# Optimization experiments

Hardware: AMD Instinct MI355X
Metric: run time of the kernel (lower is better)

Reference implementation:

```python
import jax, jax.numpy as jnp
import numpy as np

B, N, C, H = 2, 2048, 1024, 16
D = C // H  # head dim = 64
SCALE = 1.0 / (C ** 0.5)  # note: source scales by 1/sqrt(dim), not 1/sqrt(head_dim)


def setup_inputs() -> dict:
    key = jax.random.key(0)
    k1, k2, k3 = jax.random.split(key, 3)
    x = jax.random.normal(k1, (B, N, C), dtype=jnp.float32)
    w_qkv = jax.random.normal(k2, (3 * C, C), dtype=jnp.float32) * (1.0 / np.sqrt(C))
    w_proj = jax.random.normal(k3, (C, C), dtype=jnp.float32) * (1.0 / np.sqrt(C))
    b_proj = jnp.zeros((C,), dtype=jnp.float32)
    return {"x": x, "w_qkv": w_qkv, "w_proj": w_proj, "b_proj": b_proj}


def reference(x, w_qkv, w_proj, b_proj):
    Bb, Nn, Cc = x.shape
    # qkv projection (torch Linear: x @ W.T), then split into q,k,v heads
    qkv = jnp.einsum('bnc,dc->bnd', x, w_qkv)           # [B,N,3C]
    qkv = qkv.reshape(Bb, Nn, 3, H, D)
    q = qkv[:, :, 0].transpose(0, 2, 1, 3)              # [B,H,N,D]
    k = qkv[:, :, 1].transpose(0, 2, 1, 3)
    v = qkv[:, :, 2].transpose(0, 2, 1, 3)
    attn = jnp.einsum('bhnd,bhmd->bhnm', q, k) * SCALE  # [B,H,N,N]
    attn = jax.nn.softmax(attn, axis=-1)
    out = jnp.einsum('bhnm,bhmd->bhnd', attn, v)        # [B,H,N,D]
    out = out.transpose(0, 2, 1, 3).reshape(Bb, Nn, Cc)
    out = jnp.einsum('bnc,dc->bnd', out, w_proj) + b_proj
    return (out, attn)
```

## Files before the change

kernel.cpp:

```cpp
#include <hip/hip_runtime.h>

typedef __attribute__((ext_vector_type(8))) short short8;
typedef __attribute__((ext_vector_type(4))) float f32x4;
typedef __attribute__((ext_vector_type(16))) float f32x16;

#define B_ 2
#define N_ 2048
#define C_ 1024
#define H_ 16
#define SCALE_ 0.03125f

__device__ inline unsigned short f2bf(float f) {
    unsigned int u = __float_as_uint(f);
    return (unsigned short)((u + 0x7fffu + ((u >> 16) & 1u)) >> 16);
}

__device__ inline f32x4 mfma16(short8 a, short8 b, f32x4 c) {
    return __builtin_amdgcn_mfma_f32_16x16x32_bf16(a, b, c, 0, 0, 0);
}
__device__ inline f32x16 mfma32(short8 a, short8 b, f32x16 c) {
    return __builtin_amdgcn_mfma_f32_32x32x16_bf16(a, b, c, 0, 0, 0);
}

#define GLOAD_LDS16(g, l) __builtin_amdgcn_global_load_lds( \
    (const __attribute__((address_space(1))) void*)(g),     \
    (__attribute__((address_space(3))) void*)(l), 16, 0, 0)

__global__ void cvt_all(const float* __restrict__ x, const float* __restrict__ wq,
                        const float* __restrict__ wp, unsigned short* __restrict__ xb,
                        unsigned short* __restrict__ wqb, unsigned short* __restrict__ wpb) {
    int i = blockIdx.x * blockDim.x + threadIdx.x;
    const int n1 = 4096 * 1024 / 4, n2 = 3072 * 1024 / 4;
    const float* src; unsigned short* dst; int j;
    if (i < n1)            { src = x;  dst = xb;  j = i; }
    else if (i < n1 + n2)  { src = wq; dst = wqb; j = i - n1; }
    else                   { src = wp; dst = wpb; j = i - n1 - n2; }
    float4 v = *(const float4*)(src + (size_t)j * 4);
    ushort4 o;
    o.x = f2bf(v.x); o.y = f2bf(v.y); o.z = f2bf(v.z); o.w = f2bf(v.w);
    *(ushort4*)(dst + (size_t)j * 4) = o;
}

template<int BF16_OUT, int BM>
__global__ __launch_bounds__(256, 3)
void gemm_bt(const unsigned short* __restrict__ A, const unsigned short* __restrict__ Bm,
             unsigned short* __restrict__ Cb, float* __restrict__ Cf,
             const float* __restrict__ bias, int M, int N, int K,
             int xcd_cols, int bxr) {
    constexpr int AI = BM / 32;
    __shared__ unsigned short lA[BM * 64];
    __shared__ unsigned short lB[128 * 64];
    const int tid = threadIdx.x;
    const int lane = tid & 63, wave = tid >> 6;
    const int lm = lane & 15, g = lane >> 4;
    const int flat = blockIdx.x, per = gridDim.x >> 3;
    const int xcd = flat & 7, fl = flat >> 3;
    const int rpr = per / bxr;
    const int by = (xcd / xcd_cols) * rpr + fl / bxr;
    const int bx = (xcd % xcd_cols) * bxr + fl % bxr;
    const int m0 = by * BM, n0 = bx * 128;
    const int wr = wave >> 1, wc = wave & 1;

    f32x4 acc[AI][4];
    f32x4 zero = {0.f, 0.f, 0.f, 0.f};
#pragma unroll
    for (int i = 0; i < AI; ++i)
#pragma unroll
        for (int j = 0; j < 4; ++j) acc[i][j] = zero;

    const int sRow = lane >> 3;
    const int sCol = (lane & 7) * 8;

    for (int k0 = 0; k0 < K; k0 += 64) {
#pragma unroll
        for (int t = 0; t < AI; ++t) {
            int inst = wave * AI + t;
            int r = inst * 8 + sRow;
            GLOAD_LDS16(A + (size_t)(m0 + r) * K + k0 + sCol, lA + inst * 512);
        }
#pragma unroll
        for (int t = 0; t < 4; ++t) {
            int inst = wave * 4 + t;
            int r = inst * 8 + sRow;
            GLOAD_LDS16(Bm + (size_t)(n0 + r) * K + k0 + sCol, lB + inst * 512);
        }
        __syncthreads();
#pragma unroll
        for (int kk = 0; kk < 2; ++kk) {
            short8 af[AI], bfv[4];
#pragma unroll
            for (int i = 0; i < AI; ++i)
                af[i] = *(const short8*)&lA[(wr * (BM / 2) + i * 16 + lm) * 64 + kk * 32 + g * 8];
#pragma unroll
            for (int j = 0; j < 4; ++j)
                bfv[j] = *(const short8*)&lB[(wc * 64 + j * 16 + lm) * 64 + kk * 32 + g * 8];
#pragma unroll
            for (int i = 0; i < AI; ++i)
#pragma unroll
                for (int j = 0; j < 4; ++j)
                    acc[i][j] = mfma16(af[i], bfv[j], acc[i][j]);
        }
        __syncthreads();
    }
#pragma unroll
    for (int i = 0; i < AI; ++i) {
#pragma unroll
        for (int j = 0; j < 4; ++j) {
#pragma unroll
            for (int r = 0; r < 4; ++r) {
                int m = m0 + wr * (BM / 2) + i * 16 + g * 4 + r;
                int n = n0 + wc * 64 + j * 16 + lm;
                float v = acc[i][j][r];
                if (BF16_OUT)
                    Cb[(size_t)m * N + n] = f2bf(v);
                else
                    Cf[(size_t)m * N + n] = v + bias[n];
            }
        }
    }
}

__device__ inline void stage_k256(const unsigned short* kbase, unsigned short* buf, int tid) {
    const int wave = tid >> 6, lane = tid & 63;
#pragma unroll
    for (int i = 0; i < 2; ++i) {
        int c = i * 256 + wave * 64 + lane;
        int row = c >> 3, j = c & 7;
        GLOAD_LDS16(kbase + (size_t)row * 3072 + ((j ^ (row & 7)) << 3),
                    buf + (i * 256 + wave * 64) * 8);
    }
}
__device__ inline void stage_k128(const unsigned short* kbase, unsigned short* buf, int tid) {
    const int wave = tid >> 6, lane = tid & 63;
#pragma unroll
    for (int i = 0; i < 4; ++i) {
        int c = i * 128 + wave * 64 + lane;
        int row = c >> 3, j = c & 7;
        GLOAD_LDS16(kbase + (size_t)row * 3072 + ((j ^ (row & 7)) << 3),
                    buf + (i * 128 + wave * 64) * 8);
    }
}

__global__ __launch_bounds__(128, 2)
void attn_sums(const unsigned short* __restrict__ qkv, float* __restrict__ rinv_out) {
    __shared__ unsigned short kt[2 * 4096];
    const int tid = threadIdx.x, lane = tid & 63, wave = tid >> 6;
    const int l31 = lane & 31, h5 = lane >> 5, l7 = lane & 7;
    const int flat = blockIdx.x;
    const int work = ((flat & 7) << 7) | (flat >> 3);
    const int q0 = (work & 31) * 64, h = (work >> 5) & 15, b = work >> 9;
    const unsigned short* qkvB = qkv + (size_t)b * N_ * 3072;
    const unsigned short* kh = qkvB + 1024 + h * 64;

    const unsigned short* qrow = qkvB + (size_t)(q0 + wave * 32 + l31) * 3072 + h * 64;
    short8 aq[4];
#pragma unroll
    for (int ks = 0; ks < 4; ++ks) aq[ks] = *(const short8*)(qrow + ks * 16 + h5 * 8);

    float part[16];
#pragma unroll
    for (int i = 0; i < 16; ++i) part[i] = 0.f;

    stage_k128(kh, kt, tid);
    __syncthreads();

    for (int kti = 0; kti < 32; ++kti) {
        const int cur = kti & 1;
        if (kti < 31) stage_k128(kh + (size_t)(kti + 1) * 196608, kt + (cur ^ 1) * 4096, tid);
        const unsigned short* ktc = kt + cur * 4096;
        f32x16 s0 = {}, s1 = {};
        __builtin_amdgcn_s_setprio(1);
#pragma unroll
        for (int ks = 0; ks < 4; ++ks) {
            int ch = ((ks * 2 + h5) ^ l7) * 8;
            short8 b0 = *(const short8*)&ktc[l31 * 64 + ch];
            short8 b1 = *(const short8*)&ktc[(32 + l31) * 64 + ch];
            s0 = mfma32(aq[ks], b0, s0);
            s1 = mfma32(aq[ks], b1, s1);
        }
        __builtin_amdgcn_s_setprio(0);
#pragma unroll
        for (int r = 0; r < 16; ++r)
            part[r] += __expf(s0[r] * SCALE_) + __expf(s1[r] * SCALE_);
        __syncthreads();
    }
#pragma unroll
    for (int r = 0; r < 16; ++r) {
#pragma unroll
        for (int off = 1; off < 32; off <<= 1) part[r] += __shfl_xor(part[r], off);
    }
    if (l31 == 0) {
        float* base = rinv_out + (size_t)(b * H_ + h) * N_ + q0 + wave * 32 + 4 * h5;
#pragma unroll
        for (int r = 0; r < 16; ++r) base[(r & 3) + 8 * (r >> 2)] = 1.0f / part[r];
    }
}

__global__ __launch_bounds__(256, 2)
void attn_write(const unsigned short* __restrict__ qkv, const float* __restrict__ rinv_in,
                float* __restrict__ attn_out, unsigned short* __restrict__ o_out) {
    __shared__ unsigned short smem[35840];
    unsigned short* kt = smem;
    unsigned short* vt = smem + 8192;
    unsigned short* pq = smem + 17408;

    const int tid = threadIdx.x, lane = tid & 63, wave = tid >> 6;
    const int l31 = lane & 31, h5 = lane >> 5, l7 = lane & 7;
    const int flat = blockIdx.x;
    const int work = ((flat & 7) << 6) | (flat >> 3);
    const int q0 = (work & 15) * 128, h = (work >> 4) & 15, b = work >> 8;
    const unsigned short* qkvB = qkv + (size_t)b * N_ * 3072;
    const unsigned short* kh = qkvB + 1024 + h * 64;
    const unsigned short* vh = qkvB + 2048 + h * 64;

    const unsigned short* qrow = qkvB + (size_t)(q0 + wave * 32 + l31) * 3072 + h * 64;
    short8 aq[4];
#pragma unroll
    for (int ks = 0; ks < 4; ++ks) aq[ks] = *(const short8*)(qrow + ks * 16 + h5 * 8);

    float rv[16];
    {
        const float* base = rinv_in + (size_t)(b * H_ + h) * N_ + q0 + wave * 32 + 4 * h5;
#pragma unroll
        for (int r = 0; r < 16; ++r) rv[r] = base[(r & 3) + 8 * (r >> 2)];
    }

    const int rV = (tid >> 3) * 2, cV = (tid & 7) * 8;
    short8 va, vb;
#define WRITEV(buf) do { _Pragma("unroll") for (int j = 0; j < 8; ++j) { \
        int d = cV + j; int w = (rV >> 1) ^ (((d >> 3) & 7) << 2);       \
        unsigned int pk = (unsigned int)(unsigned short)va[j] |          \
                          ((unsigned int)(unsigned short)vb[j] << 16);   \
        *(unsigned int*)&vt[(buf) * 4608 + d * 72 + 2 * w] = pk; } } while (0)

    stage_k256(kh, kt, tid);
    {
        const unsigned short* sv = vh + (size_t)rV * 3072 + cV;
        va = *(const short8*)sv; vb = *(const short8*)(sv + 3072);
    }
    WRITEV(0);
    __syncthreads();

    f32x16 oa0 = {}, oa1 = {};
    float* attnB = attn_out + ((size_t)(b * H_ + h) * N_ + q0) * N_;

    for (int kti = 0; kti < 32; ++kti) {
        const int cur = kti & 1;
        if (kti < 31) {
            stage_k256(kh + (size_t)(kti + 1) * 196608, kt + (cur ^ 1) * 4096, tid);
            const unsigned short* sv = vh + (size_t)(kti + 1) * 196608 + (size_t)rV * 3072 + cV;
            va = *(const short8*)sv; vb = *(const short8*)(sv + 3072);
        }
        const unsigned short* ktc = kt + cur * 4096;
        f32x16 s0 = {}, s1 = {};
        __builtin_amdgcn_s_setprio(1);
#pragma unroll
        for (int ks = 0; ks < 4; ++ks) {
            int ch = ((ks * 2 + h5) ^ l7) * 8;
            short8 b0 = *(const short8*)&ktc[l31 * 64 + ch];
            short8 b1 = *(const short8*)&ktc[(32 + l31) * 64 + ch];
            s0 = mfma32(aq[ks], b0, s0);
            s1 = mfma32(aq[ks], b1, s1);
        }
        __builtin_amdgcn_s_setprio(0);

        float* aB = attnB + (size_t)(wave * 32 + 4 * h5) * N_ + kti * 64 + l31;
        unsigned short* pqw = pq + cur * 9216 + (wave * 32 + 4 * h5) * 72 + l31;
#pragma unroll
        for (int r = 0; r < 16; ++r) {
            int ro = (r & 3) + 8 * (r >> 2);
            float p0 = __expf(s0[r] * SCALE_) * rv[r];
            float p1 = __expf(s1[r] * SCALE_) * rv[r];
            __builtin_nontemporal_store(p0, aB + (size_t)ro * N_);
            __builtin_nontemporal_store(p1, aB + (size_t)ro * N_ + 32);
            pqw[ro * 72] = f2bf(p0);
            pqw[ro * 72 + 32] = f2bf(p1);
        }

        asm volatile("s_waitcnt vmcnt(32) lgkmcnt(0)\n\ts_barrier" ::: "memory");
        __builtin_amdgcn_sched_barrier(0);

        __builtin_amdgcn_s_setprio(1);
#pragma unroll
        for (int ks = 0; ks < 4; ++ks) {
            short8 ap = *(const short8*)&pq[cur * 9216 + (wave * 32 + l31) * 72 + ks * 16 + h5 * 8];
            int wv0 = (ks * 8 + h5 * 4) ^ (((l31 >> 3) & 7) << 2);
            short8 bv0 = *(const short8*)&vt[cur * 4608 + l31 * 72 + 2 * wv0];
            int dch = 32 + l31;
            int wv1 = (ks * 8 + h5 * 4) ^ (((dch >> 3) & 7) << 2);
            short8 bv1 = *(const short8*)&vt[cur * 4608 + dch * 72 + 2 * wv1];
            oa0 = mfma32(ap, bv0, oa0);
            oa1 = mfma32(ap, bv1, oa1);
        }
        __builtin_amdgcn_s_setprio(0);

        if (kti < 31) WRITEV(cur ^ 1);
    }

#pragma unroll
    for (int r = 0; r < 16; ++r) {
        int qrw = q0 + wave * 32 + 4 * h5 + (r & 3) + 8 * (r >> 2);
        size_t ob = (size_t)(b * N_ + qrw) * C_ + h * 64 + l31;
        o_out[ob] = f2bf(oa0[r]);
        o_out[ob + 32] = f2bf(oa1[r]);
    }
#undef WRITEV
}

extern "C" void kernel_launch(void* const* d_in, const int* in_sizes, int n_in,
                              void* d_out, int out_size, void* d_ws, size_t ws_size,
                              hipStream_t stream) {
    (void)in_sizes; (void)n_in; (void)out_size; (void)ws_size;
    const float* x      = (const float*)d_in[0];
    const float* w_qkv  = (const float*)d_in[1];
    const float* w_proj = (const float*)d_in[2];
    const float* b_proj = (const float*)d_in[3];

    float* out  = (float*)d_out;
    float* attn = out + (size_t)B_ * N_ * C_;

    unsigned short* x_b     = (unsigned short*)d_ws;
    unsigned short* wqkv_b  = x_b + (size_t)4096 * 1024;
    unsigned short* wproj_b = wqkv_b + (size_t)3072 * 1024;
    unsigned short* qkv_b   = wproj_b + (size_t)1024 * 1024;
    unsigned short* o_b     = qkv_b + (size_t)4096 * 3072;
    float* rinv = (float*)x_b;

    cvt_all<<<8192, 256, 0, stream>>>(x, w_qkv, w_proj, x_b, wqkv_b, wproj_b);

    gemm_bt<1, 128><<<768, 256, 0, stream>>>(
        x_b, wqkv_b, qkv_b, nullptr, nullptr, 4096, 3072, 1024, 2, 12);

    attn_sums<<<1024, 128, 0, stream>>>(qkv_b, rinv);
    attn_write<<<512, 256, 0, stream>>>(qkv_b, rinv, attn, o_b);

    gemm_bt<0, 64><<<512, 256, 0, stream>>>(
        o_b, wproj_b, nullptr, out, b_proj, 4096, 1024, 1024, 1, 8);
}
```

Measured before the change: 234.2 us.

## Shrink attn_write to 64-query blocks of two waves and use exp2

Changes attn_write from 256-thread blocks covering 128 queries to 128-thread blocks covering 64 queries. The grid doubles to 1024 blocks and the P staging buffer is single-buffered, cutting LDS per block so more blocks fit per CU. The V staging now loads four rows per thread. Both attention kernels replace __expf with exp2f using a pre-multiplied log2e scale. The trade-off is that each K/V tile is loaded by twice as many blocks, which adds global and L2 traffic.

```diff
diff --git a/kernel.cpp b/kernel.cpp
--- a/kernel.cpp
+++ b/kernel.cpp
@@ -9,6 +9,7 @@
 #define C_ 1024
 #define H_ 16
 #define SCALE_ 0.03125f
+#define E2SCALE_ 0.045084220f
 
 __device__ inline unsigned short f2bf(float f) {
     unsigned int u = __float_as_uint(f);
@@ -120,16 +121,6 @@
     }
 }
 
-__device__ inline void stage_k256(const unsigned short* kbase, unsigned short* buf, int tid) {
-    const int wave = tid >> 6, lane = tid & 63;
-#pragma unroll
-    for (int i = 0; i < 2; ++i) {
-        int c = i * 256 + wave * 64 + lane;
-        int row = c >> 3, j = c & 7;
-        GLOAD_LDS16(kbase + (size_t)row * 3072 + ((j ^ (row & 7)) << 3),
-                    buf + (i * 256 + wave * 64) * 8);
-    }
-}
 __device__ inline void stage_k128(const unsigned short* kbase, unsigned short* buf, int tid) {
     const int wave = tid >> 6, lane = tid & 63;
 #pragma unroll
@@ -181,7 +172,7 @@
         __builtin_amdgcn_s_setprio(0);
 #pragma unroll
         for (int r = 0; r < 16; ++r)
-            part[r] += __expf(s0[r] * SCALE_) + __expf(s1[r] * SCALE_);
+            part[r] += exp2f(s0[r] * E2SCALE_) + exp2f(s1[r] * E2SCALE_);
         __syncthreads();
     }
 #pragma unroll
@@ -196,10 +187,10 @@
     }
 }
 
-__global__ __launch_bounds__(256, 2)
+__global__ __launch_bounds__(128, 2)
 void attn_write(const unsigned short* __restrict__ qkv, const float* __restrict__ rinv_in,
                 float* __restrict__ attn_out, unsigned short* __restrict__ o_out) {
-    __shared__ unsigned short smem[35840];
+    __shared__ unsigned short smem[22016];
     unsigned short* kt = smem;
     unsigned short* vt = smem + 8192;
     unsigned short* pq = smem + 17408;
@@ -207,8 +198,8 @@
     const int tid = threadIdx.x, lane = tid & 63, wave = tid >> 6;
     const int l31 = lane & 31, h5 = lane >> 5, l7 = lane & 7;
     const int flat = blockIdx.x;
-    const int work = ((flat & 7) << 6) | (flat >> 3);
-    const int q0 = (work & 15) * 128, h = (work >> 4) & 15, b = work >> 8;
+    const int work = ((flat & 7) << 7) | (flat >> 3);
+    const int q0 = (work & 31) * 64, h = (work >> 5) & 15, b = work >> 9;
     const unsigned short* qkvB = qkv + (size_t)b * N_ * 3072;
     const unsigned short* kh = qkvB + 1024 + h * 64;
     const unsigned short* vh = qkvB + 2048 + h * 64;
@@ -225,19 +216,23 @@
         for (int r = 0; r < 16; ++r) rv[r] = base[(r & 3) + 8 * (r >> 2)];
     }
 
-    const int rV = (tid >> 3) * 2, cV = (tid & 7) * 8;
-    short8 va, vb;
-#define WRITEV(buf) do { _Pragma("unroll") for (int j = 0; j < 8; ++j) { \
-        int d = cV + j; int w = (rV >> 1) ^ (((d >> 3) & 7) << 2);       \
-        unsigned int pk = (unsigned int)(unsigned short)va[j] |          \
-                          ((unsigned int)(unsigned short)vb[j] << 16);   \
-        *(unsigned int*)&vt[(buf) * 4608 + d * 72 + 2 * w] = pk; } } while (0)
-
-    stage_k256(kh, kt, tid);
-    {
-        const unsigned short* sv = vh + (size_t)rV * 3072 + cV;
-        va = *(const short8*)sv; vb = *(const short8*)(sv + 3072);
-    }
+    const int rT = (tid >> 3) * 4, cV = (tid & 7) * 8;
+    short8 va, vb, vc, vd;
+#define LOADV(base_) do { const unsigned short* sv = (base_) + (size_t)rT * 3072 + cV; \
+        va = *(const short8*)sv; vb = *(const short8*)(sv + 3072);                     \
+        vc = *(const short8*)(sv + 6144); vd = *(const short8*)(sv + 9216); } while (0)
+#define WRITEV(buf) do { _Pragma("unroll") for (int j = 0; j < 8; ++j) {   \
+        int d = cV + j; int sw = ((d >> 3) & 7) << 2;                      \
+        int w0 = (rT >> 1) ^ sw; int w1 = ((rT >> 1) + 1) ^ sw;            \
+        unsigned int pk01 = (unsigned int)(unsigned short)va[j] |          \
+                            ((unsigned int)(unsigned short)vb[j] << 16);   \
+        unsigned int pk23 = (unsigned int)(unsigned short)vc[j] |          \
+                            ((unsigned int)(unsigned short)vd[j] << 16);   \
+        *(unsigned int*)&vt[(buf) * 4608 + d * 72 + 2 * w0] = pk01;        \
+        *(unsigned int*)&vt[(buf) * 4608 + d * 72 + 2 * w1] = pk23; } } while (0)
+
+    stage_k128(kh, kt, tid);
+    LOADV(vh);
     WRITEV(0);
     __syncthreads();
 
@@ -247,9 +242,8 @@
     for (int kti = 0; kti < 32; ++kti) {
         const int cur = kti & 1;
         if (kti < 31) {
-            stage_k256(kh + (size_t)(kti + 1) * 196608, kt + (cur ^ 1) * 4096, tid);
-            const unsigned short* sv = vh + (size_t)(kti + 1) * 196608 + (size_t)rV * 3072 + cV;
-            va = *(const short8*)sv; vb = *(const short8*)(sv + 3072);
+            stage_k128(kh + (size_t)(kti + 1) * 196608, kt + (cur ^ 1) * 4096, tid);
+            LOADV(vh + (size_t)(kti + 1) * 196608);
         }
         const unsigned short* ktc = kt + cur * 4096;
         f32x16 s0 = {}, s1 = {};
@@ -265,12 +259,12 @@
         __builtin_amdgcn_s_setprio(0);
 
         float* aB = attnB + (size_t)(wave * 32 + 4 * h5) * N_ + kti * 64 + l31;
-        unsigned short* pqw = pq + cur * 9216 + (wave * 32 + 4 * h5) * 72 + l31;
+        unsigned short* pqw = pq + (wave * 32 + 4 * h5) * 72 + l31;
 #pragma unroll
         for (int r = 0; r < 16; ++r) {
             int ro = (r & 3) + 8 * (r >> 2);
-            float p0 = __expf(s0[r] * SCALE_) * rv[r];
-            float p1 = __expf(s1[r] * SCALE_) * rv[r];
+            float p0 = exp2f(s0[r] * E2SCALE_) * rv[r];
+            float p1 = exp2f(s1[r] * E2SCALE_) * rv[r];
             __builtin_nontemporal_store(p0, aB + (size_t)ro * N_);
             __builtin_nontemporal_store(p1, aB + (size_t)ro * N_ + 32);
             pqw[ro * 72] = f2bf(p0);
@@ -283,7 +277,7 @@
         __builtin_amdgcn_s_setprio(1);
 #pragma unroll
         for (int ks = 0; ks < 4; ++ks) {
-            short8 ap = *(const short8*)&pq[cur * 9216 + (wave * 32 + l31) * 72 + ks * 16 + h5 * 8];
+            short8 ap = *(const short8*)&pq[(wave * 32 + l31) * 72 + ks * 16 + h5 * 8];
             int wv0 = (ks * 8 + h5 * 4) ^ (((l31 >> 3) & 7) << 2);
             short8 bv0 = *(const short8*)&vt[cur * 4608 + l31 * 72 + 2 * wv0];
             int dch = 32 + l31;
@@ -305,6 +299,7 @@
         o_out[ob + 32] = f2bf(oa1[r]);
     }
 #undef WRITEV
+#undef LOADV
 }
 
 extern "C" void kernel_launch(void* const* d_in, const int* in_sizes, int n_in,
@@ -332,7 +327,7 @@
         x_b, wqkv_b, qkv_b, nullptr, nullptr, 4096, 3072, 1024, 2, 12);
 
     attn_sums<<<1024, 128, 0, stream>>>(qkv_b, rinv);
-    attn_write<<<512, 256, 0, stream>>>(qkv_b, rinv, attn, o_b);
+    attn_write<<<1024, 128, 0, stream>>>(qkv_b, rinv, attn, o_b);
 
     gemm_bt<0, 64><<<512, 256, 0, stream>>>(
         o_b, wproj_b, nullptr, out, b_proj, 4096, 1024, 1024, 1, 8);
```

Result: slower. 281.1 us (+20.0%).

## Transpose QK MFMA to keep P in registers and vectorize attn stores

Applied to the files above, without the earlier changes.

Swaps the MFMA operands for S = QK^T so each lane holds one query row. The row-sum reduction then becomes a single cross-half shuffle and one rinv value per lane. In attn_write, the bf16 P fragment for the PV MFMA is built in registers using cvt_pk and permlane32_swap, instead of a round trip through LDS. The fp32 attention matrix is staged per wave in LDS and written with 16-byte nontemporal stores rather than scalar ones. This adds LDS traffic and a per-wave LDS reuse without a barrier, and it depends on permlane32_swap lane semantics being right.

```diff
diff --git a/kernel.cpp b/kernel.cpp
--- a/kernel.cpp
+++ b/kernel.cpp
@@ -3,6 +3,7 @@
 typedef __attribute__((ext_vector_type(8))) short short8;
 typedef __attribute__((ext_vector_type(4))) float f32x4;
 typedef __attribute__((ext_vector_type(16))) float f32x16;
+typedef __attribute__((ext_vector_type(4))) unsigned int u32x4;
 
 #define B_ 2
 #define N_ 2048
@@ -25,6 +26,9 @@
 #define GLOAD_LDS16(g, l) __builtin_amdgcn_global_load_lds( \
     (const __attribute__((address_space(1))) void*)(g),     \
     (__attribute__((address_space(3))) void*)(l), 16, 0, 0)
+
+#define CVTPK(d, x, y) asm("v_cvt_pk_bf16_f32 %0, %1, %2" : "=v"(d) : "v"(x), "v"(y))
+#define PLSWAP(a, b) asm volatile("v_permlane32_swap_b32 %0, %1" : "+v"(a), "+v"(b))
 
 __global__ void cvt_all(const float* __restrict__ x, const float* __restrict__ wq,
                         const float* __restrict__ wp, unsigned short* __restrict__ xb,
@@ -157,10 +161,7 @@
 #pragma unroll
     for (int ks = 0; ks < 4; ++ks) aq[ks] = *(const short8*)(qrow + ks * 16 + h5 * 8);
 
-    float part[16];
-#pragma unroll
-    for (int i = 0; i < 16; ++i) part[i] = 0.f;
-
+    float psum = 0.f;
     stage_k128(kh, kt, tid);
     __syncthreads();
 
@@ -175,34 +176,27 @@
             int ch = ((ks * 2 + h5) ^ l7) * 8;
             short8 b0 = *(const short8*)&ktc[l31 * 64 + ch];
             short8 b1 = *(const short8*)&ktc[(32 + l31) * 64 + ch];
-            s0 = mfma32(aq[ks], b0, s0);
-            s1 = mfma32(aq[ks], b1, s1);
+            s0 = mfma32(b0, aq[ks], s0);
+            s1 = mfma32(b1, aq[ks], s1);
         }
         __builtin_amdgcn_s_setprio(0);
 #pragma unroll
         for (int r = 0; r < 16; ++r)
-            part[r] += __expf(s0[r] * SCALE_) + __expf(s1[r] * SCALE_);
+            psum += __expf(s0[r] * SCALE_) + __expf(s1[r] * SCALE_);
         __syncthreads();
     }
-#pragma unroll
-    for (int r = 0; r < 16; ++r) {
-#pragma unroll
-        for (int off = 1; off < 32; off <<= 1) part[r] += __shfl_xor(part[r], off);
-    }
-    if (l31 == 0) {
-        float* base = rinv_out + (size_t)(b * H_ + h) * N_ + q0 + wave * 32 + 4 * h5;
-#pragma unroll
-        for (int r = 0; r < 16; ++r) base[(r & 3) + 8 * (r >> 2)] = 1.0f / part[r];
-    }
+    psum += __shfl_xor(psum, 32);
+    if (h5 == 0)
+        rinv_out[(size_t)(b * H_ + h) * N_ + q0 + wave * 32 + l31] = 1.0f / psum;
 }
 
 __global__ __launch_bounds__(256, 2)
 void attn_write(const unsigned short* __restrict__ qkv, const float* __restrict__ rinv_in,
                 float* __restrict__ attn_out, unsigned short* __restrict__ o_out) {
-    __shared__ unsigned short smem[35840];
+    __shared__ unsigned short smem[34816];
     unsigned short* kt = smem;
     unsigned short* vt = smem + 8192;
-    unsigned short* pq = smem + 17408;
+    float* pq32 = (float*)(smem + 17408);
 
     const int tid = threadIdx.x, lane = tid & 63, wave = tid >> 6;
     const int l31 = lane & 31, h5 = lane >> 5, l7 = lane & 7;
@@ -218,12 +212,8 @@
 #pragma unroll
     for (int ks = 0; ks < 4; ++ks) aq[ks] = *(const short8*)(qrow + ks * 16 + h5 * 8);
 
-    float rv[16];
-    {
-        const float* base = rinv_in + (size_t)(b * H_ + h) * N_ + q0 + wave * 32 + 4 * h5;
-#pragma unroll
-        for (int r = 0; r < 16; ++r) rv[r] = base[(r & 3) + 8 * (r >> 2)];
-    }
+    const float rv = rinv_in[(size_t)(b * H_ + h) * N_ + q0 + wave * 32 + l31];
+    float* pw = pq32 + wave * (32 * 68);
 
     const int rV = (tid >> 3) * 2, cV = (tid & 7) * 8;
     short8 va, vb;
@@ -243,6 +233,7 @@
 
     f32x16 oa0 = {}, oa1 = {};
     float* attnB = attn_out + ((size_t)(b * H_ + h) * N_ + q0) * N_;
+    float* aw = attnB + (size_t)(wave * 32) * N_;
 
     for (int kti = 0; kti < 32; ++kti) {
         const int cur = kti & 1;
@@ -259,31 +250,48 @@
             int ch = ((ks * 2 + h5) ^ l7) * 8;
             short8 b0 = *(const short8*)&ktc[l31 * 64 + ch];
             short8 b1 = *(const short8*)&ktc[(32 + l31) * 64 + ch];
-            s0 = mfma32(aq[ks], b0, s0);
-            s1 = mfma32(aq[ks], b1, s1);
+            s0 = mfma32(b0, aq[ks], s0);
+            s1 = mfma32(b1, aq[ks], s1);
         }
         __builtin_amdgcn_s_setprio(0);
 
-        float* aB = attnB + (size_t)(wave * 32 + 4 * h5) * N_ + kti * 64 + l31;
-        unsigned short* pqw = pq + cur * 9216 + (wave * 32 + 4 * h5) * 72 + l31;
-#pragma unroll
-        for (int r = 0; r < 16; ++r) {
-            int ro = (r & 3) + 8 * (r >> 2);
-            float p0 = __expf(s0[r] * SCALE_) * rv[r];
-            float p1 = __expf(s1[r] * SCALE_) * rv[r];
-            __builtin_nontemporal_store(p0, aB + (size_t)ro * N_);
-            __builtin_nontemporal_store(p1, aB + (size_t)ro * N_ + 32);
-            pqw[ro * 72] = f2bf(p0);
-            pqw[ro * 72 + 32] = f2bf(p1);
-        }
-
-        asm volatile("s_waitcnt vmcnt(32) lgkmcnt(0)\n\ts_barrier" ::: "memory");
+        unsigned int pb[16];
+#pragma unroll
+        for (int c4 = 0; c4 < 8; ++c4) {
+            const int rb = (c4 & 3) * 4;
+            f32x4 pc;
+            pc.x = __expf(((c4 < 4) ? s0[rb + 0] : s1[rb + 0]) * SCALE_) * rv;
+            pc.y = __expf(((c4 < 4) ? s0[rb + 1] : s1[rb + 1]) * SCALE_) * rv;
+            pc.z = __expf(((c4 < 4) ? s0[rb + 2] : s1[rb + 2]) * SCALE_) * rv;
+            pc.w = __expf(((c4 < 4) ? s0[rb + 3] : s1[rb + 3]) * SCALE_) * rv;
+            *(f32x4*)&pw[l31 * 68 + 8 * (c4 & 3) + 32 * (c4 >> 2) + 4 * h5] = pc;
+            CVTPK(pb[2 * c4], pc.x, pc.y);
+            CVTPK(pb[2 * c4 + 1], pc.z, pc.w);
+        }
+#pragma unroll
+        for (int fs = 0; fs < 4; ++fs) {
+            PLSWAP(pb[4 * fs + 0], pb[4 * fs + 2]);
+            PLSWAP(pb[4 * fs + 1], pb[4 * fs + 3]);
+        }
+#pragma unroll
+        for (int rr = 0; rr < 8; ++rr) {
+            int row = rr * 4 + (lane >> 4);
+            f32x4 rd = *(const f32x4*)&pw[row * 68 + 4 * (lane & 15)];
+            __builtin_nontemporal_store(rd,
+                (f32x4*)(aw + (size_t)row * N_ + kti * 64 + 4 * (lane & 15)));
+        }
+
+        asm volatile("s_waitcnt vmcnt(8) lgkmcnt(0)\n\ts_barrier" ::: "memory");
         __builtin_amdgcn_sched_barrier(0);
 
         __builtin_amdgcn_s_setprio(1);
 #pragma unroll
         for (int ks = 0; ks < 4; ++ks) {
-            short8 ap = *(const short8*)&pq[cur * 9216 + (wave * 32 + l31) * 72 + ks * 16 + h5 * 8];
+            short8 ap;
+            {
+                u32x4 t = {pb[4 * ks + 0], pb[4 * ks + 1], pb[4 * ks + 2], pb[4 * ks + 3]};
+                ap = *(short8*)&t;
+            }
             int wv0 = (ks * 8 + h5 * 4) ^ (((l31 >> 3) & 7) << 2);
             short8 bv0 = *(const short8*)&vt[cur * 4608 + l31 * 72 + 2 * wv0];
             int dch = 32 + l31;
```

Result: no change. 235.0 us (+0.3%).
